# Optimization experiments

Measured on AMD Instinct MI355X. Metric: run time of the kernel, lower is better.

The kernel has to match this reference:

```python
import jax, jax.numpy as jnp
import numpy as np

H = 2048  # hidden
D = 4     # bbox dims
B, T, TGT = 64, 128, 64


def lstm_cell(x, h, c, Wih, Whh, bih, bhh):
    # PyTorch gate order: i, f, g, o
    gates = x @ Wih.T + h @ Whh.T + bih + bhh  # (B, 4H)
    i, f, g, o = jnp.split(gates, 4, axis=-1)
    i = jax.nn.sigmoid(i)
    f = jax.nn.sigmoid(f)
    g = jnp.tanh(g)
    o = jax.nn.sigmoid(o)
    c_new = f * c + i * g
    h_new = o * jnp.tanh(c_new)
    return h_new, c_new


def setup_inputs() -> dict:
    key = jax.random.key(0)
    ks = jax.random.split(key, 16)
    x = jax.random.normal(ks[0], (B, T, D), dtype=jnp.float32)
    lengths = jax.random.randint(ks[1], (B,), 1, T + 1)  # valid lengths in [1, T]
    s = 1.0 / np.sqrt(H)

    def u(k, shape):
        return jax.random.uniform(k, shape, jnp.float32, -s, s)

    return dict(
        x=x, lengths=lengths, target_len=TGT,
        enc_Wih=u(ks[2], (4 * H, D)), enc_Whh=u(ks[3], (4 * H, H)),
        enc_bih=u(ks[4], (4 * H,)), enc_bhh=u(ks[5], (4 * H,)),
        emb_W=u(ks[6], (H, D)), emb_b=u(ks[7], (H,)),
        dec_Wih=u(ks[8], (4 * H, H)), dec_Whh=u(ks[9], (4 * H, H)),
        dec_bih=u(ks[10], (4 * H,)), dec_bhh=u(ks[11], (4 * H,)),
        fc_W=u(ks[12], (D, H)), fc_b=u(ks[13], (D,)),
    )


def reference(x, lengths, target_len,
              enc_Wih, enc_Whh, enc_bih, enc_bhh,
              emb_W, emb_b,
              dec_Wih, dec_Whh, dec_bih, dec_bhh,
              fc_W, fc_b):
    b, t, _ = x.shape
    # --- Encoder: LSTM over padded seq; packed semantics = freeze state past length ---
    mask = (jnp.arange(t)[:, None] < lengths[None, :])[:, :, None]  # (T, B, 1)
    xs = jnp.swapaxes(x, 0, 1)  # (T, B, D)
    h0 = jnp.zeros((b, H), x.dtype)
    c0 = jnp.zeros((b, H), x.dtype)

    def enc_step(carry, inp):
        h, c = carry
        xt, m = inp
        hn, cn = lstm_cell(xt, h, c, enc_Wih, enc_Whh, enc_bih, enc_bhh)
        return (jnp.where(m, hn, h), jnp.where(m, cn, c)), None

    (h, c), _ = jax.lax.scan(enc_step, (h0, c0), (xs, mask))

    x0 = x[jnp.arange(b), lengths - 1]  # (B, D)

    def dec_step(carry, _):
        xb, hh, cc = carry
        emb = xb @ emb_W.T + emb_b  # (B, H)
        hh, cc = lstm_cell(emb, hh, cc, dec_Wih, dec_Whh, dec_bih, dec_bhh)
        out = hh @ fc_W.T + fc_b  # (B, D)
        return (out, hh, cc), out

    (out, h, c), preds = jax.lax.scan(dec_step, (x0, h, c), None, length=target_len)
    predictions = jnp.swapaxes(preds, 0, 1)  # (B, target_len, D)
    # hidden returned with num_layers=1 leading axis, matching torch
    return predictions, out, (h[None], c[None])
```

## Files before the change

kernel.cpp:

```cpp
#include <hip/hip_runtime.h>
#include <hip/hip_fp16.h>


#define HID   2048
#define NBAT  64
#define TENC  128
#define TDEC  64
#define NBLK  256
#define NTHR  512
#define WROW  2056
#define FROW  2056

typedef _Float16 f16;
typedef _Float16 f16x8 __attribute__((ext_vector_type(8)));
typedef _Float16 f16x4 __attribute__((ext_vector_type(4)));
typedef float    f32x4v __attribute__((ext_vector_type(4)));

#define SMEM_BYTES 159936

struct Params {
  const float* x; const int* lengths;
  const float* enc_Wih; const float* enc_Whh; const float* enc_bih; const float* enc_bhh;
  const float* emb_W; const float* emb_b;
  const float* dec_Wih; const float* dec_Whh; const float* dec_bih; const float* dec_bhh;
  const float* fc_W; const float* fc_b;
  float* dst;
  f16* h16;
  unsigned* bar;
  int ring;
};

__device__ __forceinline__ void astore_u32(unsigned* p, unsigned v) {
  __hip_atomic_store(p, v, __ATOMIC_RELAXED, __HIP_MEMORY_SCOPE_AGENT);
}
__device__ __forceinline__ void astore_u64(float* p, unsigned long long v) {
  __hip_atomic_store((unsigned long long*)p, v, __ATOMIC_RELAXED, __HIP_MEMORY_SCOPE_AGENT);
}
__device__ __forceinline__ unsigned aload_u32(const unsigned* p) {
  return __hip_atomic_load(p, __ATOMIC_RELAXED, __HIP_MEMORY_SCOPE_AGENT);
}
__device__ __forceinline__ uint4 aload_u32x4(const unsigned* p) {
  uint4 r;
  asm volatile("global_load_dwordx4 %0, %1, off sc0 sc1\n\ts_waitcnt vmcnt(0)"
               : "=v"(r) : "v"(p) : "memory");
  return r;
}
__device__ __forceinline__ f16x8 bload_f16x8(const f16* p) {
  f16x8 r;
  asm volatile("global_load_dwordx4 %0, %1, off sc0 sc1" : "=v"(r) : "v"(p));
  return r;
}

__device__ __forceinline__ void ldsbar() {
  asm volatile("s_waitcnt lgkmcnt(0)" ::: "memory");
  __builtin_amdgcn_s_barrier();
}
__device__ __forceinline__ void waitpa() {
  asm volatile("s_waitcnt vmcnt(0)" ::: "memory");
  __builtin_amdgcn_sched_barrier(0);
}

__device__ __forceinline__ void gbar(unsigned* bar, unsigned& target, int bid) {
  __syncthreads();
  if (bid == 0) {
    if (threadIdx.x == 0) astore_u32(&bar[0], target);
    if (threadIdx.x < 64) {
      const unsigned* slots = bar + threadIdx.x * 4;
      for (;;) {
        uint4 v = aload_u32x4(slots);
        int ok = (v.x >= target) & (v.y >= target) & (v.z >= target) & (v.w >= target);
        if (__all(ok)) break;
        __builtin_amdgcn_s_sleep(1);
      }
      if (threadIdx.x < 32) astore_u32(&bar[512 + threadIdx.x * 32], target);
    }
  } else if (threadIdx.x == 0) {
    astore_u32(&bar[bid], target);
    while (aload_u32(&bar[512 + (bid >> 3) * 32]) < target)
      __builtin_amdgcn_s_sleep(1);
  }
  __syncthreads();
  target++;
}

__device__ __forceinline__ void fill_weights(const float* __restrict__ W, int bid,
                                             f16* wlds, int w, int l) {
  #pragma unroll
  for (int rr = 0; rr < 4; ++rr) {
    int r  = w * 4 + rr;
    int gr = ((r >> 3) << 11) + bid * 8 + (r & 7);
    const float4* src = (const float4*)(W + (size_t)gr * HID);
    f16* dst = wlds + (size_t)r * WROW;
    #pragma unroll
    for (int it = 0; it < 8; ++it) {
      float4 v = src[it * 64 + l];
      f16x4 h4; h4[0] = (f16)v.x; h4[1] = (f16)v.y; h4[2] = (f16)v.z; h4[3] = (f16)v.w;
      *(f16x4*)(dst + (it * 64 + l) * 4) = h4;
    }
  }
}

__device__ __forceinline__ void gemm_prefetch(const f16* __restrict__ hp, int ring,
                                              int w, int l15, int quad,
                                              f16x8* pa0, f16x8* pa1) {
  const int mh = w & 1, kq = w >> 1;
  const f16* A0 = hp + (size_t)(mh * 32 + l15) * HID + kq * 512 + quad * 8;
  const f16* A1 = A0 + (size_t)16 * HID;
  if (ring) {
    #pragma unroll
    for (int ch = 0; ch < 16; ++ch) {
      pa0[ch] = *(const f16x8*)(A0 + ch * 32);
      pa1[ch] = *(const f16x8*)(A1 + ch * 32);
    }
  } else {
    #pragma unroll
    for (int ch = 0; ch < 16; ++ch) {
      pa0[ch] = bload_f16x8(A0 + ch * 32);
      pa1[ch] = bload_f16x8(A1 + ch * 32);
    }
  }
}

__device__ __forceinline__ void fc_compute(const f16* fcT, float* fcp,
                                           int w, int l15, int quad,
                                           const f16x8* pa0, const f16x8* pa1) {
  const int mh = w & 1, kq = w >> 1;
  f32x4v f0 = {0.f, 0.f, 0.f, 0.f}, f1 = f0;
  const f16* BF = fcT + (size_t)l15 * FROW + kq * 512 + quad * 8;
  #pragma unroll
  for (int ch = 0; ch < 16; ++ch) {
    f16x8 vbF = {};
    if (l15 < 4) vbF = *(const f16x8*)(BF + ch * 32);
    f0 = __builtin_amdgcn_mfma_f32_16x16x32_f16(pa0[ch], vbF, f0, 0, 0, 0);
    f1 = __builtin_amdgcn_mfma_f32_16x16x32_f16(pa1[ch], vbF, f1, 0, 0, 0);
  }
  if (l15 < 4) {
    const int brow = mh * 32 + quad * 4;
    #pragma unroll
    for (int r = 0; r < 4; ++r) {
      unsafeAtomicAdd(&fcp[(brow + r) * 4 + l15],      f0[r]);
      unsafeAtomicAdd(&fcp[(brow + 16 + r) * 4 + l15], f1[r]);
    }
  }
}

template<bool FC>
__device__ __forceinline__ void gemm_compute(const f16* wlds, const f16* fcT,
                                             float* gbuf, float* fcp,
                                             int w, int l15, int quad,
                                             const f16x8* pa0, const f16x8* pa1) {
  const int mh = w & 1, kq = w >> 1;
  f32x4v a00 = {0.f, 0.f, 0.f, 0.f}, a01 = a00, a10 = a00, a11 = a00;
  const f16* B0 = wlds + (size_t)l15 * WROW + kq * 512 + quad * 8;
  const f16* B1 = B0 + (size_t)16 * WROW;
  #pragma unroll
  for (int ch = 0; ch < 16; ++ch) {
    f16x8 vb0 = *(const f16x8*)(B0 + ch * 32);
    f16x8 vb1 = *(const f16x8*)(B1 + ch * 32);
    a00 = __builtin_amdgcn_mfma_f32_16x16x32_f16(pa0[ch], vb0, a00, 0, 0, 0);
    a01 = __builtin_amdgcn_mfma_f32_16x16x32_f16(pa0[ch], vb1, a01, 0, 0, 0);
    a10 = __builtin_amdgcn_mfma_f32_16x16x32_f16(pa1[ch], vb0, a10, 0, 0, 0);
    a11 = __builtin_amdgcn_mfma_f32_16x16x32_f16(pa1[ch], vb1, a11, 0, 0, 0);
  }
  const int brow = mh * 32 + quad * 4;
  #pragma unroll
  for (int r = 0; r < 4; ++r) {
    unsafeAtomicAdd(&gbuf[(brow + r)      * 36 +      l15], a00[r]);
    unsafeAtomicAdd(&gbuf[(brow + r)      * 36 + 16 + l15], a01[r]);
    unsafeAtomicAdd(&gbuf[(brow + 16 + r) * 36 +      l15], a10[r]);
    unsafeAtomicAdd(&gbuf[(brow + 16 + r) * 36 + 16 + l15], a11[r]);
  }
  if (FC) fc_compute(fcT, fcp, w, l15, quad, pa0, pa1);
}

extern "C" __global__ void __launch_bounds__(NTHR, 2)
lstm_persistent(Params P) {
  extern __shared__ char smem[];
  f16*   wlds = (f16*)smem;
  float* gbuf = (float*)(smem + 131584);
  float* xv   = (float*)(smem + 140800);
  float* wsm  = (float*)(smem + 141824);
  float* bsm  = (float*)(smem + 142336);
  float* fcp  = (float*)(smem + 142464);
  f16*   fcT  = (f16*)(smem + 143488);

  const int t    = threadIdx.x;
  const int bid  = blockIdx.x;
  const int w    = t >> 6;
  const int l    = t & 63;
  const int l15  = l & 15;
  const int quad = l >> 4;
  const int bb   = t >> 3;
  const int jj   = t & 7;
  const int jglob = bid * 8 + jj;
  const int ring = P.ring;
  const size_t GEN = (size_t)NBAT * HID;

  unsigned target = 1;

  if (t == 0)
    asm volatile("s_waitcnt vmcnt(0)\n\tbuffer_inv sc0 sc1\n\ts_waitcnt vmcnt(0)" ::: "memory");
  __syncthreads();

  if (t < 32) {
    int r = t, gr = ((r >> 3) << 11) + bid * 8 + (r & 7);
    ((float4*)wsm)[r] = ((const float4*)P.enc_Wih)[gr];
    bsm[r] = P.enc_bih[gr] + P.enc_bhh[gr];
  }
  fill_weights(P.enc_Whh, bid, wlds, w, l);

  const int len_b = P.lengths[bb];
  const float4 fcb = ((const float4*)P.fc_b)[0];
  float hreg = 0.f, creg = 0.f;

  for (int ts = 0; ts < TENC; ++ts) {
    const size_t roff = (size_t)(ring ? ts : (ts & 1)) * GEN;
    const size_t woff = (size_t)(ring ? (ts + 1) : ((ts + 1) & 1)) * GEN;
    float4 xvv;
    if (t < NBAT) xvv = ((const float4*)P.x)[t * TENC + ts];
    f16x8 pa0[16], pa1[16];
    if (ts > 0) gemm_prefetch(P.h16 + roff, ring, w, l15, quad, pa0, pa1);
    if (t < NBAT) ((float4*)xv)[t] = xvv;
    ldsbar();
    for (int e = t; e < 2048; e += NTHR) {
      int b = e >> 5, n = e & 31;
      float4 wv = ((const float4*)wsm)[n];
      const float* xb = xv + b * 4;
      gbuf[b * 36 + n] = bsm[n] + xb[0] * wv.x + xb[1] * wv.y + xb[2] * wv.z + xb[3] * wv.w;
    }
    ldsbar();
    if (ts > 0) { waitpa(); gemm_compute<false>(wlds, fcT, gbuf, fcp, w, l15, quad, pa0, pa1); }
    ldsbar();
    {
      float gi = gbuf[bb * 36 + jj],      gf = gbuf[bb * 36 + 8 + jj];
      float gg = gbuf[bb * 36 + 16 + jj], go = gbuf[bb * 36 + 24 + jj];
      float ii = 1.f / (1.f + expf(-gi));
      float ff = 1.f / (1.f + expf(-gf));
      float g  = tanhf(gg);
      float oo = 1.f / (1.f + expf(-go));
      float cn = ff * creg + ii * g;
      float hn = oo * tanhf(cn);
      if (ts < len_b) { creg = cn; hreg = hn; }
      unsigned hv = (unsigned)__builtin_bit_cast(unsigned short, (f16)hreg);
      unsigned v1 = __shfl_down(hv, 1), v2 = __shfl_down(hv, 2), v3 = __shfl_down(hv, 3);
      if ((t & 3) == 0) {
        unsigned long long pk = (unsigned long long)hv | ((unsigned long long)v1 << 16)
                              | ((unsigned long long)v2 << 32) | ((unsigned long long)v3 << 48);
        astore_u64((float*)(P.h16 + woff + (size_t)bb * HID + bid * 8 + (jj & 4)), pk);
      }
    }
    gbar(P.bar, target, bid);
  }

  fill_weights(P.dec_Whh, bid, wlds, w, l);
  #pragma unroll
  for (int rr = 0; rr < 4; ++rr) {
    int r = w * 4 + rr, gr = ((r >> 3) << 11) + bid * 8 + (r & 7);
    const float* wr = P.dec_Wih + (size_t)gr * HID;
    float a0 = 0.f, a1 = 0.f, a2 = 0.f, a3 = 0.f, ab = 0.f;
    for (int k = l; k < HID; k += 64) {
      float wv = wr[k];
      float4 e = ((const float4*)P.emb_W)[k];
      a0 += wv * e.x; a1 += wv * e.y; a2 += wv * e.z; a3 += wv * e.w;
      ab += wv * P.emb_b[k];
    }
    #pragma unroll
    for (int off = 32; off > 0; off >>= 1) {
      a0 += __shfl_xor(a0, off); a1 += __shfl_xor(a1, off);
      a2 += __shfl_xor(a2, off); a3 += __shfl_xor(a3, off);
      ab += __shfl_xor(ab, off);
    }
    if (l == 0) {
      wsm[r * 4 + 0] = a0; wsm[r * 4 + 1] = a1; wsm[r * 4 + 2] = a2; wsm[r * 4 + 3] = a3;
      bsm[r] = ab + P.dec_bih[gr] + P.dec_bhh[gr];
    }
  }
  for (int i = t; i < 2048; i += NTHR) {
    int d = i >> 9, k4 = i & 511;
    float4 v = ((const float4*)P.fc_W)[i];
    f16x4 h4; h4[0] = (f16)v.x; h4[1] = (f16)v.y; h4[2] = (f16)v.z; h4[3] = (f16)v.w;
    *(f16x4*)(fcT + (size_t)d * FROW + k4 * 4) = h4;
  }
  ldsbar();

  for (int s = 0; s < TDEC; ++s) {
    const int rgen = TENC + s, wgen = rgen + 1;
    const size_t roff = (size_t)(ring ? rgen : (rgen & 1)) * GEN;
    const size_t woff = (size_t)(ring ? wgen : (wgen & 1)) * GEN;
    f16x8 pa0[16], pa1[16];
    gemm_prefetch(P.h16 + roff, ring, w, l15, quad, pa0, pa1);
    if (t < 256) fcp[t] = 0.f;
    for (int e = t; e < 2048; e += NTHR) {
      int b = e >> 5, n = e & 31;
      gbuf[b * 36 + n] = bsm[n];
    }
    ldsbar();
    waitpa();
    gemm_compute<true>(wlds, fcT, gbuf, fcp, w, l15, quad, pa0, pa1);
    ldsbar();
    if (t < NBAT) {
      float4 o;
      if (s == 0) {
        o = ((const float4*)P.x)[t * TENC + (P.lengths[t] - 1)];
      } else {
        float4 p = ((const float4*)fcp)[t];
        o.x = fcb.x + p.x; o.y = fcb.y + p.y; o.z = fcb.z + p.z; o.w = fcb.w + p.w;
      }
      ((float4*)xv)[t] = o;
      if (s >= 1 && bid == s)
        ((float4*)P.dst)[t * TDEC + (s - 1)] = o;
    }
    ldsbar();
    for (int e = t; e < 2048; e += NTHR) {
      int b = e >> 5, n = e & 31;
      float4 wv = ((const float4*)wsm)[n];
      const float* xb = xv + b * 4;
      gbuf[b * 36 + n] += xb[0] * wv.x + xb[1] * wv.y + xb[2] * wv.z + xb[3] * wv.w;
    }
    ldsbar();
    {
      float gi = gbuf[bb * 36 + jj],      gf = gbuf[bb * 36 + 8 + jj];
      float gg = gbuf[bb * 36 + 16 + jj], go = gbuf[bb * 36 + 24 + jj];
      float ii = 1.f / (1.f + expf(-gi));
      float ff = 1.f / (1.f + expf(-gf));
      float g  = tanhf(gg);
      float oo = 1.f / (1.f + expf(-go));
      creg = ff * creg + ii * g;
      hreg = oo * tanhf(creg);
      unsigned hv = (unsigned)__builtin_bit_cast(unsigned short, (f16)hreg);
      unsigned v1 = __shfl_down(hv, 1), v2 = __shfl_down(hv, 2), v3 = __shfl_down(hv, 3);
      if ((t & 3) == 0) {
        unsigned long long pk = (unsigned long long)hv | ((unsigned long long)v1 << 16)
                              | ((unsigned long long)v2 << 32) | ((unsigned long long)v3 << 48);
        astore_u64((float*)(P.h16 + woff + (size_t)bb * HID + bid * 8 + (jj & 4)), pk);
      }
    }
    gbar(P.bar, target, bid);
  }

  if (bid == 0) {
    if (t < 256) fcp[t] = 0.f;
    f16x8 pa0[16], pa1[16];
    gemm_prefetch(P.h16 + (size_t)(ring ? (TENC + TDEC) : ((TENC + TDEC) & 1)) * GEN,
                  ring, w, l15, quad, pa0, pa1);
    ldsbar();
    waitpa();
    fc_compute(fcT, fcp, w, l15, quad, pa0, pa1);
    ldsbar();
    if (t < NBAT) {
      float4 p = ((const float4*)fcp)[t];
      float4 o;
      o.x = fcb.x + p.x; o.y = fcb.y + p.y; o.z = fcb.z + p.z; o.w = fcb.w + p.w;
      ((float4*)P.dst)[t * TDEC + 63] = o;
      ((float4*)(P.dst + 16384))[t]   = o;
    }
  }
  P.dst[16640  + (size_t)bb * HID + jglob] = hreg;
  P.dst[147712 + (size_t)bb * HID + jglob] = creg;
}

extern "C" void kernel_launch(void* const* d_in, const int* in_sizes, int n_in,
                              void* d_out, int out_size, void* d_ws, size_t ws_size,
                              hipStream_t stream) {
  (void)in_sizes; (void)n_in; (void)out_size;
  Params P;
  P.x        = (const float*)d_in[0];
  P.lengths  = (const int*)  d_in[1];
  P.enc_Wih  = (const float*)d_in[3];
  P.enc_Whh  = (const float*)d_in[4];
  P.enc_bih  = (const float*)d_in[5];
  P.enc_bhh  = (const float*)d_in[6];
  P.emb_W    = (const float*)d_in[7];
  P.emb_b    = (const float*)d_in[8];
  P.dec_Wih  = (const float*)d_in[9];
  P.dec_Whh  = (const float*)d_in[10];
  P.dec_bih  = (const float*)d_in[11];
  P.dec_bhh  = (const float*)d_in[12];
  P.fc_W     = (const float*)d_in[13];
  P.fc_b     = (const float*)d_in[14];
  P.dst      = (float*)d_out;

  char* ws = (char*)d_ws;
  const size_t slot = (size_t)NBAT * HID * sizeof(_Float16);
  const size_t ring_bytes = (size_t)(TENC + TDEC + 1) * slot;
  int ring = (ws_size >= ring_bytes + 16384) ? 1 : 0;
  P.h16  = (f16*)ws;
  P.bar  = (unsigned*)(ws + (ring ? ring_bytes : 2 * slot));
  P.ring = ring;

  hipMemsetAsync(P.bar, 0, 12288, stream);

  hipFuncSetAttribute((const void*)lstm_persistent,
                      hipFuncAttributeMaxDynamicSharedMemorySize, SMEM_BYTES);
  void* args[] = { &P };
  hipLaunchCooperativeKernel((const void*)lstm_persistent, dim3(NBLK), dim3(NTHR),
                             args, SMEM_BYTES, stream);
}
```

Before: 4.302 ms.

## Replace global barrier with per-slice dataflow flags and block-major h layout

Drops the centralized two-level grid barrier. Each block now publishes a per-step arrival flag, and each wave polls only the 64 producer flags covering the K-slice it reads, so consumers can start as soon as their inputs are ready. The h16 buffer is relaid out block-major so each slice maps to a contiguous producer range. The input projection is folded into the gate evaluation, which removes an LDS pass and a barrier. The risks are more polling traffic, and memory-ordering correctness with the non-ring double buffer, since there is no longer a full barrier preventing overwrite races.

```diff
diff --git a/kernel.cpp b/kernel.cpp
--- a/kernel.cpp
+++ b/kernel.cpp
@@ -17,6 +17,8 @@
 typedef float    f32x4v __attribute__((ext_vector_type(4)));
 
 #define SMEM_BYTES 159936
+
+#define DOT4(a,b) ((a).x*(b).x + (a).y*(b).y + (a).z*(b).z + (a).w*(b).w)
 
 struct Params {
   const float* x; const int* lengths;
@@ -30,27 +32,14 @@
   int ring;
 };
 
-__device__ __forceinline__ void astore_u32(unsigned* p, unsigned v) {
-  __hip_atomic_store(p, v, __ATOMIC_RELAXED, __HIP_MEMORY_SCOPE_AGENT);
-}
-__device__ __forceinline__ void astore_u64(float* p, unsigned long long v) {
+__device__ __forceinline__ void astore_u64(f16* p, unsigned long long v) {
   __hip_atomic_store((unsigned long long*)p, v, __ATOMIC_RELAXED, __HIP_MEMORY_SCOPE_AGENT);
-}
-__device__ __forceinline__ unsigned aload_u32(const unsigned* p) {
-  return __hip_atomic_load(p, __ATOMIC_RELAXED, __HIP_MEMORY_SCOPE_AGENT);
-}
-__device__ __forceinline__ uint4 aload_u32x4(const unsigned* p) {
-  uint4 r;
-  asm volatile("global_load_dwordx4 %0, %1, off sc0 sc1\n\ts_waitcnt vmcnt(0)"
-               : "=v"(r) : "v"(p) : "memory");
-  return r;
 }
 __device__ __forceinline__ f16x8 bload_f16x8(const f16* p) {
   f16x8 r;
   asm volatile("global_load_dwordx4 %0, %1, off sc0 sc1" : "=v"(r) : "v"(p));
   return r;
 }
-
 __device__ __forceinline__ void ldsbar() {
   asm volatile("s_waitcnt lgkmcnt(0)" ::: "memory");
   __builtin_amdgcn_s_barrier();
@@ -60,27 +49,21 @@
   __builtin_amdgcn_sched_barrier(0);
 }
 
-__device__ __forceinline__ void gbar(unsigned* bar, unsigned& target, int bid) {
-  __syncthreads();
-  if (bid == 0) {
-    if (threadIdx.x == 0) astore_u32(&bar[0], target);
-    if (threadIdx.x < 64) {
-      const unsigned* slots = bar + threadIdx.x * 4;
-      for (;;) {
-        uint4 v = aload_u32x4(slots);
-        int ok = (v.x >= target) & (v.y >= target) & (v.z >= target) & (v.w >= target);
-        if (__all(ok)) break;
-        __builtin_amdgcn_s_sleep(1);
-      }
-      if (threadIdx.x < 32) astore_u32(&bar[512 + threadIdx.x * 32], target);
-    }
-  } else if (threadIdx.x == 0) {
-    astore_u32(&bar[bid], target);
-    while (aload_u32(&bar[512 + (bid >> 3) * 32]) < target)
-      __builtin_amdgcn_s_sleep(1);
-  }
-  __syncthreads();
-  target++;
+__device__ __forceinline__ void wait_slice(const unsigned* bar, int kq, int l,
+                                           unsigned level) {
+  const unsigned* slot = bar + (kq << 6) + l;
+  for (;;) {
+    unsigned v;
+    asm volatile("global_load_dword %0, %1, off sc0 sc1\n\ts_waitcnt vmcnt(0)"
+                 : "=v"(v) : "v"(slot) : "memory");
+    if (v >= level) break;
+    __builtin_amdgcn_s_sleep(1);
+  }
+}
+__device__ __forceinline__ void arrive(unsigned* bar, int bid, unsigned level) {
+  asm volatile("s_waitcnt vmcnt(0)" ::: "memory");
+  asm volatile("global_store_dword %0, %1, off sc0 sc1\n\ts_waitcnt vmcnt(0)"
+               :: "v"(bar + bid), "v"(level) : "memory");
 }
 
 __device__ __forceinline__ void fill_weights(const float* __restrict__ W, int bid,
@@ -104,19 +87,18 @@
                                               int w, int l15, int quad,
                                               f16x8* pa0, f16x8* pa1) {
   const int mh = w & 1, kq = w >> 1;
-  const f16* A0 = hp + (size_t)(mh * 32 + l15) * HID + kq * 512 + quad * 8;
-  const f16* A1 = A0 + (size_t)16 * HID;
+  const f16* A0 = hp + ((size_t)(kq * 64 + quad)) * 512 + (size_t)(mh * 32 + l15) * 8;
   if (ring) {
     #pragma unroll
     for (int ch = 0; ch < 16; ++ch) {
-      pa0[ch] = *(const f16x8*)(A0 + ch * 32);
-      pa1[ch] = *(const f16x8*)(A1 + ch * 32);
+      pa0[ch] = *(const f16x8*)(A0 + ch * 2048);
+      pa1[ch] = *(const f16x8*)(A0 + ch * 2048 + 128);
     }
   } else {
     #pragma unroll
     for (int ch = 0; ch < 16; ++ch) {
-      pa0[ch] = bload_f16x8(A0 + ch * 32);
-      pa1[ch] = bload_f16x8(A1 + ch * 32);
+      pa0[ch] = bload_f16x8(A0 + ch * 2048);
+      pa1[ch] = bload_f16x8(A0 + ch * 2048 + 128);
     }
   }
 }
@@ -190,14 +172,13 @@
   const int l    = t & 63;
   const int l15  = l & 15;
   const int quad = l >> 4;
+  const int kq   = w >> 1;
   const int bb   = t >> 3;
   const int jj   = t & 7;
   const int jglob = bid * 8 + jj;
   const int ring = P.ring;
   const size_t GEN = (size_t)NBAT * HID;
 
-  unsigned target = 1;
-
   if (t == 0)
     asm volatile("s_waitcnt vmcnt(0)\n\tbuffer_inv sc0 sc1\n\ts_waitcnt vmcnt(0)" ::: "memory");
   __syncthreads();
@@ -216,24 +197,27 @@
   for (int ts = 0; ts < TENC; ++ts) {
     const size_t roff = (size_t)(ring ? ts : (ts & 1)) * GEN;
     const size_t woff = (size_t)(ring ? (ts + 1) : ((ts + 1) & 1)) * GEN;
-    float4 xvv;
-    if (t < NBAT) xvv = ((const float4*)P.x)[t * TENC + ts];
+    if (ts > 0) wait_slice(P.bar, kq, l, (unsigned)ts);
     f16x8 pa0[16], pa1[16];
     if (ts > 0) gemm_prefetch(P.h16 + roff, ring, w, l15, quad, pa0, pa1);
-    if (t < NBAT) ((float4*)xv)[t] = xvv;
-    ldsbar();
+    if (t < NBAT) ((float4*)xv)[t] = ((const float4*)P.x)[t * TENC + ts];
     for (int e = t; e < 2048; e += NTHR) {
       int b = e >> 5, n = e & 31;
-      float4 wv = ((const float4*)wsm)[n];
-      const float* xb = xv + b * 4;
-      gbuf[b * 36 + n] = bsm[n] + xb[0] * wv.x + xb[1] * wv.y + xb[2] * wv.z + xb[3] * wv.w;
+      gbuf[b * 36 + n] = bsm[n];
     }
     ldsbar();
     if (ts > 0) { waitpa(); gemm_compute<false>(wlds, fcT, gbuf, fcp, w, l15, quad, pa0, pa1); }
     ldsbar();
     {
-      float gi = gbuf[bb * 36 + jj],      gf = gbuf[bb * 36 + 8 + jj];
-      float gg = gbuf[bb * 36 + 16 + jj], go = gbuf[bb * 36 + 24 + jj];
+      const float4 xb  = ((const float4*)xv)[bb];
+      const float4 wi4 = ((const float4*)wsm)[jj];
+      const float4 wf4 = ((const float4*)wsm)[8 + jj];
+      const float4 wg4 = ((const float4*)wsm)[16 + jj];
+      const float4 wo4 = ((const float4*)wsm)[24 + jj];
+      float gi = gbuf[bb * 36 + jj]      + DOT4(xb, wi4);
+      float gf = gbuf[bb * 36 + 8 + jj]  + DOT4(xb, wf4);
+      float gg = gbuf[bb * 36 + 16 + jj] + DOT4(xb, wg4);
+      float go = gbuf[bb * 36 + 24 + jj] + DOT4(xb, wo4);
       float ii = 1.f / (1.f + expf(-gi));
       float ff = 1.f / (1.f + expf(-gf));
       float g  = tanhf(gg);
@@ -246,10 +230,11 @@
       if ((t & 3) == 0) {
         unsigned long long pk = (unsigned long long)hv | ((unsigned long long)v1 << 16)
                               | ((unsigned long long)v2 << 32) | ((unsigned long long)v3 << 48);
-        astore_u64((float*)(P.h16 + woff + (size_t)bb * HID + bid * 8 + (jj & 4)), pk);
+        astore_u64(P.h16 + woff + (size_t)bid * 512 + (size_t)bb * 8 + (jj & 4), pk);
       }
     }
-    gbar(P.bar, target, bid);
+    __syncthreads();
+    if (t == 0) arrive(P.bar, bid, (unsigned)(ts + 1));
   }
 
   fill_weights(P.dec_Whh, bid, wlds, w, l);
@@ -287,6 +272,7 @@
     const int rgen = TENC + s, wgen = rgen + 1;
     const size_t roff = (size_t)(ring ? rgen : (rgen & 1)) * GEN;
     const size_t woff = (size_t)(ring ? wgen : (wgen & 1)) * GEN;
+    wait_slice(P.bar, kq, l, (unsigned)rgen);
     f16x8 pa0[16], pa1[16];
     gemm_prefetch(P.h16 + roff, ring, w, l15, quad, pa0, pa1);
     if (t < 256) fcp[t] = 0.f;
@@ -311,16 +297,16 @@
         ((float4*)P.dst)[t * TDEC + (s - 1)] = o;
     }
     ldsbar();
-    for (int e = t; e < 2048; e += NTHR) {
-      int b = e >> 5, n = e & 31;
-      float4 wv = ((const float4*)wsm)[n];
-      const float* xb = xv + b * 4;
-      gbuf[b * 36 + n] += xb[0] * wv.x + xb[1] * wv.y + xb[2] * wv.z + xb[3] * wv.w;
-    }
-    ldsbar();
     {
-      float gi = gbuf[bb * 36 + jj],      gf = gbuf[bb * 36 + 8 + jj];
-      float gg = gbuf[bb * 36 + 16 + jj], go = gbuf[bb * 36 + 24 + jj];
+      const float4 xb  = ((const float4*)xv)[bb];
+      const float4 wi4 = ((const float4*)wsm)[jj];
+      const float4 wf4 = ((const float4*)wsm)[8 + jj];
+      const float4 wg4 = ((const float4*)wsm)[16 + jj];
+      const float4 wo4 = ((const float4*)wsm)[24 + jj];
+      float gi = gbuf[bb * 36 + jj]      + DOT4(xb, wi4);
+      float gf = gbuf[bb * 36 + 8 + jj]  + DOT4(xb, wf4);
+      float gg = gbuf[bb * 36 + 16 + jj] + DOT4(xb, wg4);
+      float go = gbuf[bb * 36 + 24 + jj] + DOT4(xb, wo4);
       float ii = 1.f / (1.f + expf(-gi));
       float ff = 1.f / (1.f + expf(-gf));
       float g  = tanhf(gg);
@@ -332,13 +318,15 @@
       if ((t & 3) == 0) {
         unsigned long long pk = (unsigned long long)hv | ((unsigned long long)v1 << 16)
                               | ((unsigned long long)v2 << 32) | ((unsigned long long)v3 << 48);
-        astore_u64((float*)(P.h16 + woff + (size_t)bb * HID + bid * 8 + (jj & 4)), pk);
+        astore_u64(P.h16 + woff + (size_t)bid * 512 + (size_t)bb * 8 + (jj & 4), pk);
       }
     }
-    gbar(P.bar, target, bid);
+    __syncthreads();
+    if (t == 0) arrive(P.bar, bid, (unsigned)wgen);
   }
 
   if (bid == 0) {
+    wait_slice(P.bar, kq, l, (unsigned)(TENC + TDEC));
     if (t < 256) fcp[t] = 0.f;
     f16x8 pa0[16], pa1[16];
     gemm_prefetch(P.h16 + (size_t)(ring ? (TENC + TDEC) : ((TENC + TDEC) & 1)) * GEN,
```

Result: faster. 4.048 ms (-5.9%).
